# Optimization experiments

Measured on AMD Instinct MI355X. Metric: run time of the kernel, lower is better.

## Reference

```python
import jax, jax.numpy as jnp
import numpy as np

D_MODEL = 1024
HEAD_SIZE = 128
SCALE = float(np.sqrt(HEAD_SIZE))


def setup_inputs() -> dict:
    key = jax.random.key(0)
    kx, kq, kk, kv = jax.random.split(key, 4)
    B, T = 4, 4096
    x = jax.random.normal(kx, (B, T, D_MODEL), dtype=jnp.float32)
    # torch nn.Linear(d_model, head_size, bias=False) weight: [head_size, d_model]
    s = 1.0 / np.sqrt(D_MODEL)
    Wq = jax.random.uniform(kq, (HEAD_SIZE, D_MODEL), jnp.float32, -s, s)
    Wk = jax.random.uniform(kk, (HEAD_SIZE, D_MODEL), jnp.float32, -s, s)
    Wv = jax.random.uniform(kv, (HEAD_SIZE, D_MODEL), jnp.float32, -s, s)
    return {"x": x, "Wq": Wq, "Wk": Wk, "Wv": Wv}


def reference(x, Wq, Wk, Wv):
    B, T, C = x.shape
    q = jnp.einsum('btc,hc->bth', x, Wq)  # [B,T,hs]
    k = jnp.einsum('btc,hc->bth', x, Wk)
    v = jnp.einsum('btc,hc->bth', x, Wv)
    scores = jnp.einsum('bth,bsh->bts', q, k) / SCALE  # [B,T,T]
    causal = jnp.tril(jnp.ones((T, T), dtype=bool))
    scores = jnp.where(causal, scores, -jnp.inf)
    attn = jax.nn.softmax(scores, axis=-1)
    # dropout p=0.0 -> identity
    return jnp.einsum('bts,bsh->bth', attn, v)
```

## Files before the change

### kernel.cpp

```cpp
#include <hip/hip_runtime.h>


typedef __attribute__((ext_vector_type(8))) short short8;
typedef __attribute__((ext_vector_type(8))) unsigned short ushort8;
typedef __attribute__((ext_vector_type(4))) unsigned short ushort4v;
typedef __attribute__((ext_vector_type(4))) float f32x4;
typedef __attribute__((ext_vector_type(16))) float f32x16;
typedef __attribute__((ext_vector_type(4))) int int4v;
typedef unsigned int u32;
typedef unsigned short u16;

#define MFMA32(a, b, c) __builtin_amdgcn_mfma_f32_32x32x16_bf16((a), (b), (c), 0, 0, 0)
#define WAITVM0() asm volatile("s_waitcnt vmcnt(0)" ::: "memory")
#define NEG_INF (-1e30f)

__device__ __forceinline__ void gload16(const void* g, void* l) {
  __builtin_amdgcn_global_load_lds((const __attribute__((address_space(1))) u32*)g,
                                   (__attribute__((address_space(3))) u32*)l, 16, 0, 0);
}

__device__ __forceinline__ u16 f2bf(float f) {
  u32 u = __builtin_bit_cast(u32, f);
  u = u + 0x7FFFu + ((u >> 16) & 1u);
  return (u16)(u >> 16);
}

__device__ __forceinline__ u32 cvtpk(float lo, float hi) {
  u32 r;
  asm("v_cvt_pk_bf16_f32 %0, %1, %2" : "=v"(r) : "v"(lo), "v"(hi));
  return r;
}

__device__ __forceinline__ short8 cvt8(const float* p) {
  float4 a = *(const float4*)p;
  float4 b = *(const float4*)(p + 4);
  short8 v;
  v[0] = (short)f2bf(a.x); v[1] = (short)f2bf(a.y);
  v[2] = (short)f2bf(a.z); v[3] = (short)f2bf(a.w);
  v[4] = (short)f2bf(b.x); v[5] = (short)f2bf(b.y);
  v[6] = (short)f2bf(b.z); v[7] = (short)f2bf(b.w);
  return v;
}

__global__ __launch_bounds__(256) void wconv_kernel(const float* __restrict__ Wq,
                                                    const float* __restrict__ Wk,
                                                    const float* __restrict__ Wv,
                                                    u16* __restrict__ Wb) {
  int g = (blockIdx.x * 256 + threadIdx.x) * 8;
  const float* src;
  if (g < 131072)      src = Wq + g;
  else if (g < 262144) src = Wk + (g - 131072);
  else                 src = Wv + (g - 262144);
  float4 a = *(const float4*)src;
  float4 b = *(const float4*)(src + 4);
  ushort8 o;
  o[0] = f2bf(a.x); o[1] = f2bf(a.y); o[2] = f2bf(a.z); o[3] = f2bf(a.w);
  o[4] = f2bf(b.x); o[5] = f2bf(b.y); o[6] = f2bf(b.z); o[7] = f2bf(b.w);
  *(ushort8*)(Wb + g) = o;
}

#define QK_SCALE 0.127517446f

__global__ __launch_bounds__(512, 1) void qkv_proj_kernel(const float* __restrict__ x,
                                                          const u16* __restrict__ Wb,
                                                          u16* __restrict__ qout,
                                                          u16* __restrict__ kout,
                                                          u16* __restrict__ vtout) {
  __shared__ __align__(16) unsigned char Wlds[2][49152];
  const int tid = threadIdx.x;
  const int w = tid >> 6;
  const int l = tid & 63;
  const int h = l >> 5, n32 = l & 31;
  const int mh = w >> 2, ng = w & 3;
  const int m0 = (int)blockIdx.x * 64 + mh * 32;

  f32x16 acc[3];
#pragma unroll
  for (int j = 0; j < 3; ++j)
#pragma unroll
    for (int r = 0; r < 16; ++r) acc[j][r] = 0.f;

  const float* xrow = x + (size_t)(m0 + n32) * 1024;

#define STAGE_W(buf, ks)                                                       \
  {                                                                            \
    _Pragma("unroll") for (int c = 0; c < 6; ++c) {                            \
      int L = c * 512 + tid;                                                   \
      int row = L >> 3, chp = L & 7;                                           \
      int gch = chp ^ (row & 7);                                               \
      gload16((const char*)Wb + row * 2048 + (ks) * 128 + gch * 16,            \
              (unsigned char*)Wlds[buf] + c * 8192 + w * 1024);                \
    }                                                                          \
  }

  STAGE_W(0, 0);
  int cur = 0;
  for (int ks = 0; ks < 16; ++ks) {
    WAITVM0();
    __builtin_amdgcn_s_barrier();
    __builtin_amdgcn_sched_barrier(0);
    if (ks < 15) STAGE_W(cur ^ 1, ks + 1);
    const char* base0 = (const char*)Wlds[cur];
    __builtin_amdgcn_s_setprio(1);
#pragma unroll
    for (int k16 = 0; k16 < 4; ++k16) {
      short8 a = cvt8(xrow + ks * 64 + k16 * 16 + h * 8);
#pragma unroll
      for (int j = 0; j < 3; ++j) {
        int nrow = (ng * 3 + j) * 32 + n32;
        short8 b = *(const short8*)(base0 + nrow * 128 +
                                    ((k16 * 32 + h * 16) ^ ((nrow & 7) << 4)));
        acc[j] = MFMA32(a, b, acc[j]);
      }
    }
    __builtin_amdgcn_s_setprio(0);
    cur ^= 1;
  }
#undef STAGE_W

#pragma unroll
  for (int j = 0; j < 3; ++j) {
    int ti = ng * 3 + j;
    int gcol = ti * 32 + n32;
    if (ti < 4) {
#pragma unroll
      for (int r = 0; r < 16; ++r) {
        int row = m0 + (r & 3) + 8 * (r >> 2) + 4 * h;
        qout[(size_t)row * 128 + gcol] = f2bf(acc[j][r] * QK_SCALE);
      }
    } else if (ti < 8) {
#pragma unroll
      for (int r = 0; r < 16; ++r) {
        int row = m0 + (r & 3) + 8 * (r >> 2) + 4 * h;
        kout[(size_t)row * 128 + (gcol - 128)] = f2bf(acc[j][r]);
      }
    } else {
      int d = gcol - 256;
#pragma unroll
      for (int rq = 0; rq < 4; ++rq) {
        int t0 = m0 + rq * 8 + 4 * h;
        ushort4v o4;
#pragma unroll
        for (int i = 0; i < 4; ++i) o4[i] = f2bf(acc[j][rq * 4 + i]);
        *(ushort4v*)&vtout[(size_t)((t0 >> 12) * 128 + d) * 4096 + (t0 & 4095)] = o4;
      }
    }
  }
}

template <int NSPLIT>
__global__ __launch_bounds__(256, 2) void attn_kernel(const u16* __restrict__ qws,
                                                      const u16* __restrict__ kws,
                                                      const u16* __restrict__ vtws,
                                                      float* __restrict__ out,
                                                      float* __restrict__ opart,
                                                      float* __restrict__ mlpart) {
  __shared__ __align__(16) unsigned char Klds[2][16384];
  __shared__ __align__(16) unsigned char Vlds[2][16384];

  const int tid = threadIdx.x;
  const int w = tid >> 6;
  const int l = tid & 63;
  const int h = l >> 5, q32 = l & 31;
  const int bid = (int)blockIdx.x;
  const int sp = bid & (NSPLIT - 1);
  const int tb = bid / NSPLIT;
  const int bi = tb & 3;
  const int qt = 31 - (tb >> 2);
  const int q0w = qt * 128 + w * 32;
  const int grow = bi * 4096 + q0w + q32;
  const int qg = q0w + q32;

  const int nsteps = 2 * qt + 2;
  const int s_lo = (nsteps * sp) / NSPLIT;
  const int s_hi = (nsteps * (sp + 1)) / NSPLIT;

  if constexpr (NSPLIT > 1) {
    if (s_lo >= s_hi) {
      if (h == 0) {
        mlpart[sp * 16384 + grow] = NEG_INF;
        mlpart[NSPLIT * 16384 + sp * 16384 + grow] = 0.f;
      }
      return;
    }
  }

  short8 qf[8];
  const u16* qp = qws + (size_t)grow * 128 + h * 8;
#pragma unroll
  for (int ks = 0; ks < 8; ++ks) qf[ks] = *(const short8*)(qp + ks * 16);

  f32x16 ot[4];
#pragma unroll
  for (int dt = 0; dt < 4; ++dt)
#pragma unroll
    for (int r = 0; r < 16; ++r) ot[dt][r] = 0.f;
  float mreg = NEG_INF, lsum = 0.f;

  const char* kbatch = (const char*)kws + (size_t)bi * 4096 * 256;
  const char* vbatch = (const char*)vtws + (size_t)bi * 128 * 8192;

#define STAGE_KV(buf, kv0)                                                     \
  {                                                                            \
    _Pragma("unroll") for (int c = 0; c < 4; ++c) {                            \
      int L = c * 256 + tid;                                                   \
      int row = L >> 4, chp = L & 15;                                          \
      int gch = chp ^ (row & 7);                                               \
      gload16(kbatch + (size_t)((kv0) + row) * 256 + gch * 16,                 \
              (unsigned char*)Klds[buf] + c * 4096 + w * 1024);                \
    }                                                                          \
    _Pragma("unroll") for (int c = 0; c < 4; ++c) {                            \
      int L = c * 256 + tid;                                                   \
      int row = L >> 3, chp = L & 7;                                           \
      int gch = chp ^ (row & 7);                                               \
      gload16(vbatch + (size_t)row * 8192 + (size_t)(kv0) * 2 + gch * 16,      \
              (unsigned char*)Vlds[buf] + c * 4096 + w * 1024);                \
    }                                                                          \
  }

  STAGE_KV(0, s_lo * 64);
  int cur = 0;

  for (int s = s_lo; s < s_hi; ++s) {
    WAITVM0();
    __builtin_amdgcn_s_barrier();
    __builtin_amdgcn_sched_barrier(0);
    if (s + 1 < s_hi) STAGE_KV(cur ^ 1, (s + 1) * 64);
    const int kv0 = s * 64;
    const bool active = (kv0 <= q0w + 31);

    if (active) {
      f32x16 st0, st1;
#pragma unroll
      for (int r = 0; r < 16; ++r) { st0[r] = 0.f; st1[r] = 0.f; }
      const char* Kb = (const char*)Klds[cur];
      const int sw = (q32 & 7) << 4;
      __builtin_amdgcn_s_setprio(1);
#pragma unroll
      for (int ks = 0; ks < 8; ++ks) {
        int coff = ks * 32 + h * 16;
        short8 a0 = *(const short8*)(Kb + q32 * 256 + (coff ^ sw));
        st0 = MFMA32(a0, qf[ks], st0);
        short8 a1 = *(const short8*)(Kb + (32 + q32) * 256 + (coff ^ sw));
        st1 = MFMA32(a1, qf[ks], st1);
      }
      __builtin_amdgcn_s_setprio(0);

      if (kv0 + 63 > q0w) {
#pragma unroll
        for (int r = 0; r < 16; ++r) {
          int kvr = kv0 + (r & 3) + 8 * (r >> 2) + 4 * h;
          if (kvr > qg) st0[r] = NEG_INF;
          if (kvr + 32 > qg) st1[r] = NEG_INF;
        }
      }

      float tmax = st0[0];
#pragma unroll
      for (int r = 1; r < 16; ++r) tmax = fmaxf(tmax, st0[r]);
#pragma unroll
      for (int r = 0; r < 16; ++r) tmax = fmaxf(tmax, st1[r]);
      tmax = fmaxf(tmax, __shfl_xor(tmax, 32));
      if (!__all(tmax <= mreg + 8.0f)) {
        float mnew = fmaxf(mreg, tmax);
        float alpha = exp2f(mreg - mnew);
        lsum *= alpha;
#pragma unroll
        for (int dt = 0; dt < 4; ++dt)
#pragma unroll
          for (int r = 0; r < 16; ++r) ot[dt][r] *= alpha;
        mreg = mnew;
      }
      float rs = 0.f;
#pragma unroll
      for (int r = 0; r < 16; ++r) { st0[r] = exp2f(st0[r] - mreg); rs += st0[r]; }
#pragma unroll
      for (int r = 0; r < 16; ++r) { st1[r] = exp2f(st1[r] - mreg); rs += st1[r]; }
      rs += __shfl_xor(rs, 32);
      lsum += rs;

      const char* Vb = (const char*)Vlds[cur];
      __builtin_amdgcn_s_setprio(1);
#pragma unroll
      for (int t = 0; t < 4; ++t) {
        const f32x16& stt = (t < 2) ? st0 : st1;
        const int rb = (t & 1) * 8;
        u32 A0 = cvtpk(stt[rb + 0], stt[rb + 1]);
        u32 C0 = cvtpk(stt[rb + 2], stt[rb + 3]);
        u32 B0 = cvtpk(stt[rb + 4], stt[rb + 5]);
        u32 D0 = cvtpk(stt[rb + 6], stt[rb + 7]);
        u32 Ax = (u32)__shfl_xor((int)A0, 32);
        u32 Bx = (u32)__shfl_xor((int)B0, 32);
        u32 Cx = (u32)__shfl_xor((int)C0, 32);
        u32 Dx = (u32)__shfl_xor((int)D0, 32);
        int4v pbv;
        pbv[0] = (int)(h ? Bx : A0);
        pbv[1] = (int)(h ? Dx : C0);
        pbv[2] = (int)(h ? B0 : Ax);
        pbv[3] = (int)(h ? D0 : Cx);
        short8 pb = __builtin_bit_cast(short8, pbv);
#pragma unroll
        for (int dt = 0; dt < 4; ++dt) {
          int row = dt * 32 + q32;
          short8 va = *(const short8*)(Vb + row * 128 + ((t * 32 + h * 16) ^ sw));
          ot[dt] = MFMA32(va, pb, ot[dt]);
        }
      }
      __builtin_amdgcn_s_setprio(0);
    }
    cur ^= 1;
  }

  if constexpr (NSPLIT == 1) {
    float inv = 1.0f / lsum;
    float* ob = out + (size_t)grow * 128;
#pragma unroll
    for (int dt = 0; dt < 4; ++dt)
#pragma unroll
      for (int rq = 0; rq < 4; ++rq) {
        f32x4 v4;
#pragma unroll
        for (int i = 0; i < 4; ++i) v4[i] = ot[dt][rq * 4 + i] * inv;
        *(f32x4*)(ob + dt * 32 + rq * 8 + 4 * h) = v4;
      }
  } else {
    float* ob = opart + ((size_t)sp * 16384 + grow) * 128;
#pragma unroll
    for (int dt = 0; dt < 4; ++dt)
#pragma unroll
      for (int rq = 0; rq < 4; ++rq) {
        f32x4 v4;
#pragma unroll
        for (int i = 0; i < 4; ++i) v4[i] = ot[dt][rq * 4 + i];
        *(f32x4*)(ob + dt * 32 + rq * 8 + 4 * h) = v4;
      }
    if (h == 0) {
      mlpart[sp * 16384 + grow] = mreg;
      mlpart[NSPLIT * 16384 + sp * 16384 + grow] = lsum;
    }
  }
#undef STAGE_KV
}

__global__ __launch_bounds__(256) void combine_kernel(const float* __restrict__ opart,
                                                      const float* __restrict__ mlpart,
                                                      float* __restrict__ out) {
  int idx = blockIdx.x * 256 + threadIdx.x;
  int row = idx >> 7;
  float m0 = mlpart[row], m1 = mlpart[16384 + row];
  float m2 = mlpart[32768 + row], m3 = mlpart[49152 + row];
  float M = fmaxf(fmaxf(m0, m1), fmaxf(m2, m3));
  float s0 = exp2f(m0 - M), s1 = exp2f(m1 - M);
  float s2 = exp2f(m2 - M), s3 = exp2f(m3 - M);
  const float* lp = mlpart + 65536;
  float L = lp[row] * s0 + lp[16384 + row] * s1 + lp[32768 + row] * s2 + lp[49152 + row] * s3;
  size_t o = (size_t)idx;
  float O = opart[o] * s0 + opart[o + 2097152] * s1 +
            opart[o + 4194304] * s2 + opart[o + 6291456] * s3;
  out[o] = O / L;
}

extern "C" void kernel_launch(void* const* d_in, const int* in_sizes, int n_in,
                              void* d_out, int out_size, void* d_ws, size_t ws_size,
                              hipStream_t stream) {
  (void)in_sizes; (void)n_in; (void)out_size;
  const float* x  = (const float*)d_in[0];
  const float* Wq = (const float*)d_in[1];
  const float* Wk = (const float*)d_in[2];
  const float* Wv = (const float*)d_in[3];
  float* out = (float*)d_out;
  char* ws = (char*)d_ws;
  u16* qws  = (u16*)(ws);
  u16* kws  = (u16*)(ws + (4u << 20));
  u16* vtws = (u16*)(ws + (8u << 20));
  u16* Wb   = (u16*)(ws + (12u << 20));
  float* opart  = (float*)(ws + (13u << 20));
  float* mlpart = (float*)(ws + (47u << 20));

  wconv_kernel<<<dim3(192), dim3(256), 0, stream>>>(Wq, Wk, Wv, Wb);
  qkv_proj_kernel<<<dim3(256), dim3(512), 0, stream>>>(x, Wb, qws, kws, vtws);
  if (ws_size >= ((size_t)48 << 20)) {
    attn_kernel<4><<<dim3(512), dim3(256), 0, stream>>>(qws, kws, vtws, nullptr, opart, mlpart);
    combine_kernel<<<dim3(8192), dim3(256), 0, stream>>>(opart, mlpart, out);
  } else {
    attn_kernel<1><<<dim3(128), dim3(256), 0, stream>>>(qws, kws, vtws, out, nullptr, nullptr);
  }
}
```

Before: 109.4 us.

## Stage bf16-converted x tiles in LDS shared across waves in QKV projection

The QKV projection used to have each wave load its x rows from global memory and convert them to bf16 on its own. The four N-group waves sharing the same rows therefore repeated those loads and conversions. Now each thread loads one 8-float slice per K step, converts it with packed cvt instructions and writes it to a swizzled double-buffered LDS tile that all waves read as MFMA A-operands. The next slice is prefetched in registers, the explicit vmcnt wait is replaced by __syncthreads, and the launch-bounds occupancy hint is raised to 2 blocks per CU. The changes add LDS traffic and a register cap, and correctness of the LDS-DMA wait now depends on the barrier's implicit waitcnt.

```diff
diff --git a/kernel.cpp b/kernel.cpp
--- a/kernel.cpp
+++ b/kernel.cpp
@@ -29,17 +29,6 @@
   u32 r;
   asm("v_cvt_pk_bf16_f32 %0, %1, %2" : "=v"(r) : "v"(lo), "v"(hi));
   return r;
-}
-
-__device__ __forceinline__ short8 cvt8(const float* p) {
-  float4 a = *(const float4*)p;
-  float4 b = *(const float4*)(p + 4);
-  short8 v;
-  v[0] = (short)f2bf(a.x); v[1] = (short)f2bf(a.y);
-  v[2] = (short)f2bf(a.z); v[3] = (short)f2bf(a.w);
-  v[4] = (short)f2bf(b.x); v[5] = (short)f2bf(b.y);
-  v[6] = (short)f2bf(b.z); v[7] = (short)f2bf(b.w);
-  return v;
 }
 
 __global__ __launch_bounds__(256) void wconv_kernel(const float* __restrict__ Wq,
@@ -61,26 +50,30 @@
 
 #define QK_SCALE 0.127517446f
 
-__global__ __launch_bounds__(512, 1) void qkv_proj_kernel(const float* __restrict__ x,
+__global__ __launch_bounds__(512, 2) void qkv_proj_kernel(const float* __restrict__ x,
                                                           const u16* __restrict__ Wb,
                                                           u16* __restrict__ qout,
                                                           u16* __restrict__ kout,
                                                           u16* __restrict__ vtout) {
   __shared__ __align__(16) unsigned char Wlds[2][49152];
+  __shared__ __align__(16) unsigned char Xlds[2][8192];
   const int tid = threadIdx.x;
   const int w = tid >> 6;
   const int l = tid & 63;
   const int h = l >> 5, n32 = l & 31;
   const int mh = w >> 2, ng = w & 3;
-  const int m0 = (int)blockIdx.x * 64 + mh * 32;
+  const int m0 = (int)blockIdx.x * 64;
+
+  const int xr = tid >> 3, xc = tid & 7;
+  const float* xsrc = x + (size_t)(m0 + xr) * 1024 + xc * 8;
+  unsigned char* const xw0 = (unsigned char*)Xlds[0] + xr * 128 + ((xc * 16) ^ ((xr & 7) << 4));
+  unsigned char* const xw1 = (unsigned char*)Xlds[1] + xr * 128 + ((xc * 16) ^ ((xr & 7) << 4));
 
   f32x16 acc[3];
 #pragma unroll
   for (int j = 0; j < 3; ++j)
 #pragma unroll
     for (int r = 0; r < 16; ++r) acc[j][r] = 0.f;
-
-  const float* xrow = x + (size_t)(m0 + n32) * 1024;
 
 #define STAGE_W(buf, ks)                                                       \
   {                                                                            \
@@ -93,22 +86,37 @@
     }                                                                          \
   }
 
+  float4 xa = *(const float4*)(xsrc);
+  float4 xb = *(const float4*)(xsrc + 4);
   STAGE_W(0, 0);
+
+  const int am = mh * 32 + n32;
+  const int asw = (am & 7) << 4;
   int cur = 0;
+
   for (int ks = 0; ks < 16; ++ks) {
-    WAITVM0();
-    __builtin_amdgcn_s_barrier();
-    __builtin_amdgcn_sched_barrier(0);
-    if (ks < 15) STAGE_W(cur ^ 1, ks + 1);
-    const char* base0 = (const char*)Wlds[cur];
+    int4v xv;
+    xv[0] = (int)cvtpk(xa.x, xa.y);
+    xv[1] = (int)cvtpk(xa.z, xa.w);
+    xv[2] = (int)cvtpk(xb.x, xb.y);
+    xv[3] = (int)cvtpk(xb.z, xb.w);
+    *(int4v*)(cur ? xw1 : xw0) = xv;
+    __syncthreads();
+    if (ks < 15) {
+      xa = *(const float4*)(xsrc + (ks + 1) * 64);
+      xb = *(const float4*)(xsrc + (ks + 1) * 64 + 4);
+      STAGE_W(cur ^ 1, ks + 1);
+    }
+    const char* xb0 = (const char*)Xlds[cur];
+    const char* wb0 = (const char*)Wlds[cur];
     __builtin_amdgcn_s_setprio(1);
 #pragma unroll
     for (int k16 = 0; k16 < 4; ++k16) {
-      short8 a = cvt8(xrow + ks * 64 + k16 * 16 + h * 8);
+      short8 a = *(const short8*)(xb0 + am * 128 + ((k16 * 32 + h * 16) ^ asw));
 #pragma unroll
       for (int j = 0; j < 3; ++j) {
         int nrow = (ng * 3 + j) * 32 + n32;
-        short8 b = *(const short8*)(base0 + nrow * 128 +
+        short8 b = *(const short8*)(wb0 + nrow * 128 +
                                     ((k16 * 32 + h * 16) ^ ((nrow & 7) << 4)));
         acc[j] = MFMA32(a, b, acc[j]);
       }
@@ -118,6 +126,7 @@
   }
 #undef STAGE_W
 
+  const int m0e = m0 + mh * 32;
 #pragma unroll
   for (int j = 0; j < 3; ++j) {
     int ti = ng * 3 + j;
@@ -125,20 +134,20 @@
     if (ti < 4) {
 #pragma unroll
       for (int r = 0; r < 16; ++r) {
-        int row = m0 + (r & 3) + 8 * (r >> 2) + 4 * h;
+        int row = m0e + (r & 3) + 8 * (r >> 2) + 4 * h;
         qout[(size_t)row * 128 + gcol] = f2bf(acc[j][r] * QK_SCALE);
       }
     } else if (ti < 8) {
 #pragma unroll
       for (int r = 0; r < 16; ++r) {
-        int row = m0 + (r & 3) + 8 * (r >> 2) + 4 * h;
+        int row = m0e + (r & 3) + 8 * (r >> 2) + 4 * h;
         kout[(size_t)row * 128 + (gcol - 128)] = f2bf(acc[j][r]);
       }
     } else {
       int d = gcol - 256;
 #pragma unroll
       for (int rq = 0; rq < 4; ++rq) {
-        int t0 = m0 + rq * 8 + 4 * h;
+        int t0 = m0e + rq * 8 + 4 * h;
         ushort4v o4;
 #pragma unroll
         for (int i = 0; i < 4; ++i) o4[i] = f2bf(acc[j][rq * 4 + i]);
```

After: 91.69 us. -16.2%, faster.
